# Kernel optimization log

Measured on AMD Instinct MI355X. Metric: run time of the kernel, lower is better.

## Reference

```python
import jax, jax.numpy as jnp
import numpy as np

OUT_C, IN_C, KS, KN = 256, 256, 3, 4
TEMP = 1.0
D1 = OUT_C * KS            # 768
D2 = IN_C * KS             # 768
D2R = D2 // 2 + 1          # 385 (rfft width)


def _freq_indices():
    # mirror torch get_fft2freq(d1, d2, use_rfft=True)
    fh = np.fft.fftfreq(D1)
    fw = np.fft.rfftfreq(D2)
    grid = np.stack(np.meshgrid(fh, fw, indexing='ij'), axis=-1)  # (D1, D2R, 2)
    dist = np.linalg.norm(grid, axis=-1).ravel()
    idx = np.argsort(dist, kind='stable')
    return (idx // D2R).astype(np.int32), (idx % D2R).astype(np.int32)


def setup_inputs() -> dict:
    key = jax.random.key(0)
    k1, k2, k3 = jax.random.split(key, 3)
    b, h, w = 8, 64, 64
    fh, fw = _freq_indices()
    num_freq = fh.shape[0]  # 295680 = D1 * D2R (param_reduction == 1.0)
    return {
        'x': jax.random.normal(k1, (b, IN_C, h, w), dtype=jnp.float32),
        'dft_weight': jax.random.normal(k2, (KN, num_freq, 2), dtype=jnp.float32) * 1e-6,
        'k_att': jax.random.normal(k3, (b, KN, 1, 1), dtype=jnp.float32),
        'freq_h': jnp.asarray(fh),
        'freq_w': jnp.asarray(fw),
    }


def reference(x, dft_weight, k_att, freq_h, freq_w):
    b, c, h, w = x.shape
    # kernel attention: sigmoid(att / temp) * 2 / kernel_num
    att = jax.nn.sigmoid(k_att / TEMP) * (2.0 / KN)          # (b, KN, 1, 1)
    # weighted sum of per-kernel frequency weights -> (b, F, 2)
    wsum = jnp.einsum('knf,bk->bnf', dft_weight, att.reshape(b, KN))
    wc = jax.lax.complex(wsum[..., 0], wsum[..., 1])          # (b, F) complex
    # scatter into dense rfft2 map (indices are a permutation: no duplicates)
    dft_map = jnp.zeros((b, D1, D2R), dtype=jnp.complex64)
    dft_map = dft_map.at[:, freq_h, freq_w].set(wc)
    # inverse rFFT2 -> spatial weights (b, D1, D2)
    sw = jnp.fft.irfft2(dft_map, s=(D1, D2))
    # (b, out, ks, in, ks) -> (b, out, in, ks, ks) -> grouped-conv kernel
    wk = sw.reshape(b, OUT_C, KS, IN_C, KS).transpose(0, 1, 3, 2, 4)
    wk = wk.reshape(b * OUT_C, IN_C, KS, KS)
    # batch of per-sample convs == one grouped conv with groups=b
    xg = x.reshape(1, b * c, h, w)
    out = jax.lax.conv_general_dilated(
        xg, wk, window_strides=(1, 1), padding=[(1, 1), (1, 1)],
        dimension_numbers=('NCHW', 'OIHW', 'NCHW'), feature_group_count=b)
    return out.reshape(b, OUT_C, out.shape[2], out.shape[3])
```

## Files before the change

kernel.cpp:

```cpp
#include <hip/hip_runtime.h>
#include <math.h>

#define D1 768
#define D2R 385
#define NF 295680
#define KNUM 4
#define NB 8
#define NC 256
#define TWOPI_768 0.008181230868723419f

#define ATW_U32 1572864u
#define YA_U32 2752512u
#define T_U32 3981312u
#define SPECB_K_U32 344064u
#define WBF_BYTE 9437184u

typedef __attribute__((ext_vector_type(8))) short short8;
typedef __attribute__((ext_vector_type(16))) float f32x16;
union U4S8 { unsigned int u[4]; uint4 u4; short8 s8; };

static __device__ __forceinline__ unsigned int f2bf(float f) {
  unsigned int u = __float_as_uint(f);
  return (u + 0x7fffu + ((u >> 16) & 1u)) >> 16;
}

__global__ __launch_bounds__(256) void prep_kernel(
    const float* __restrict__ dw, const int* __restrict__ fh,
    const int* __restrict__ fw, unsigned int* __restrict__ ws) {
  long i = (long)blockIdx.x * 256 + threadIdx.x;
  if (i < 1182720) {
    int k = (int)(i / NF);
    int r = (int)(i - (long)k * NF);
    const float2 v = ((const float2*)dw)[i];
    int h = fh[r], c = fw[r];
    ws[(size_t)k * SPECB_K_U32 + (size_t)c * 768 + h] =
        f2bf(v.x) | (f2bf(v.y) << 16);
    return;
  }
  long j = i - 1182720;
  if (j < 1179648) {
    int ri = (int)(j / 589824);
    int rem = (int)(j - (long)ri * 589824);
    int m = rem / 768, h = rem - (rem / 768) * 768;
    int idx = (h * m) % 768;
    float s, c;
    sincosf((float)idx * TWOPI_768, &s, &c);
    unsigned lo, hi;
    if (ri == 0) { lo = f2bf(c); hi = f2bf(-s); }
    else         { lo = f2bf(s); hi = f2bf(c); }
    ws[ATW_U32 + j] = lo | (hi << 16);
  } else if (j < 1486848) {
    long p = j - 1179648;
    int n = (int)(p / 400), cc = (int)(p - (p / 400) * 400);
    unsigned v = 0;
    if (cc <= 384) {
      float wgt = (cc == 0 || cc == 384) ? 1.6954210069444445e-6f
                                         : 3.390842013888889e-6f;
      int idx = (cc * n) % 768;
      float s, c;
      sincosf((float)idx * TWOPI_768, &s, &c);
      v = f2bf(wgt * c) | (f2bf(-wgt * s) << 16);
    }
    ws[T_U32 + (size_t)n * 400 + cc] = v;
  } else if (j < 1680384) {
    long p = j - 1486848;
    int k = (int)(p / 48384);
    long r = p - (long)k * 48384;
    int row = 385 + (int)(r / 768);
    int col = (int)(r - (r / 768) * 768);
    ws[(size_t)k * SPECB_K_U32 + (size_t)row * 768 + col] = 0u;
  } else if (j < 1726464) {
    long p = j - 1680384;
    int k = (int)(p / 11520);
    long r = p - (long)k * 11520;
    int m = (int)(r / 15), jj = (int)(r - (r / 15) * 15);
    ws[YA_U32 + (size_t)k * 307200 + (size_t)m * 400 + 385 + jj] = 0u;
  }
}

__global__ __launch_bounds__(256) void fftA_kernel(
    const unsigned short* __restrict__ Atw,
    const unsigned short* __restrict__ specB,
    unsigned short* __restrict__ Ya) {
  __shared__ __align__(16) unsigned short Al[2][64 * 40], Bl[2][64 * 40];
  int t = threadIdx.x;
  int mt = blockIdx.x, nt = blockIdx.y, z = blockIdx.z;
  int ri = z & 1, k = z >> 1;
  const unsigned short* Ag =
      Atw + (size_t)ri * 1179648 + (size_t)(mt * 64) * 1536;
  const unsigned short* Bg =
      specB + (size_t)k * 688128 + (size_t)(nt * 64) * 1536;
  int rowS = t >> 2, q = t & 3;
  int lane = t & 63, w = t >> 6;
  int moff = (w & 1) * 32, noff = (w >> 1) * 32;
  int lm = lane & 31, half = lane >> 5;
  int wr = rowS * 40 + q * 8;
  int ao = (moff + lm) * 40 + half * 8;
  int bo = (noff + lm) * 40 + half * 8;

  f32x16 acc;
#pragma unroll
  for (int r = 0; r < 16; ++r) acc[r] = 0.f;

  uint4 av = *(const uint4*)(Ag + (size_t)rowS * 1536 + q * 8);
  uint4 bv = *(const uint4*)(Bg + (size_t)rowS * 1536 + q * 8);
  *(uint4*)&Al[0][wr] = av;
  *(uint4*)&Bl[0][wr] = bv;
  __syncthreads();

  for (int kb = 0; kb < 48; ++kb) {
    bool more = (kb < 47);
    if (more) {
      av = *(const uint4*)(Ag + (size_t)rowS * 1536 + (kb + 1) * 32 + q * 8);
      bv = *(const uint4*)(Bg + (size_t)rowS * 1536 + (kb + 1) * 32 + q * 8);
    }
    const unsigned short* Ab = Al[kb & 1];
    const unsigned short* Bb = Bl[kb & 1];
#pragma unroll
    for (int kk2 = 0; kk2 < 2; ++kk2) {
      short8 a8 = *(const short8*)&Ab[ao + kk2 * 16];
      short8 b8 = *(const short8*)&Bb[bo + kk2 * 16];
      acc = __builtin_amdgcn_mfma_f32_32x32x16_bf16(a8, b8, acc, 0, 0, 0);
    }
    if (more) {
      *(uint4*)&Al[(kb + 1) & 1][wr] = av;
      *(uint4*)&Bl[(kb + 1) & 1][wr] = bv;
    }
    __syncthreads();
  }

  int c = nt * 64 + noff + lm;
  if (c < D2R) {
    unsigned short* Yk = Ya + (size_t)k * 614400;
    int mb = mt * 64 + moff + 4 * half;
#pragma unroll
    for (int reg = 0; reg < 16; ++reg) {
      int m = mb + (reg & 3) + 8 * (reg >> 2);
      Yk[(size_t)m * 800 + 2 * c + ri] = (unsigned short)f2bf(acc[reg]);
    }
  }
}

__global__ __launch_bounds__(256) void fftB_kernel(
    const unsigned short* __restrict__ Ya, const unsigned short* __restrict__ T,
    float* __restrict__ SW) {
  __shared__ __align__(16) unsigned short Al[2][64 * 40], Bl[2][64 * 40];
  int t = threadIdx.x;
  int mt = blockIdx.x, nt = blockIdx.y, k = blockIdx.z;
  const unsigned short* Ag = Ya + (size_t)k * 614400 + (size_t)(mt * 64) * 800;
  const unsigned short* Bg = T + (size_t)(nt * 64) * 800;
  int rowS = t >> 2, q = t & 3;
  int lane = t & 63, w = t >> 6;
  int moff = (w & 1) * 32, noff = (w >> 1) * 32;
  int lm = lane & 31, half = lane >> 5;
  int wr = rowS * 40 + q * 8;
  int ao = (moff + lm) * 40 + half * 8;
  int bo = (noff + lm) * 40 + half * 8;

  f32x16 acc;
#pragma unroll
  for (int r = 0; r < 16; ++r) acc[r] = 0.f;

  uint4 av = *(const uint4*)(Ag + (size_t)rowS * 800 + q * 8);
  uint4 bv = *(const uint4*)(Bg + (size_t)rowS * 800 + q * 8);
  *(uint4*)&Al[0][wr] = av;
  *(uint4*)&Bl[0][wr] = bv;
  __syncthreads();

  for (int kb = 0; kb < 25; ++kb) {
    bool more = (kb < 24);
    if (more) {
      av = *(const uint4*)(Ag + (size_t)rowS * 800 + (kb + 1) * 32 + q * 8);
      bv = *(const uint4*)(Bg + (size_t)rowS * 800 + (kb + 1) * 32 + q * 8);
    }
    const unsigned short* Ab = Al[kb & 1];
    const unsigned short* Bb = Bl[kb & 1];
#pragma unroll
    for (int kk2 = 0; kk2 < 2; ++kk2) {
      short8 a8 = *(const short8*)&Ab[ao + kk2 * 16];
      short8 b8 = *(const short8*)&Bb[bo + kk2 * 16];
      acc = __builtin_amdgcn_mfma_f32_32x32x16_bf16(a8, b8, acc, 0, 0, 0);
    }
    if (more) {
      *(uint4*)&Al[(kb + 1) & 1][wr] = av;
      *(uint4*)&Bl[(kb + 1) & 1][wr] = bv;
    }
    __syncthreads();
  }

  float* SWk = SW + (size_t)k * 589824;
  int n = nt * 64 + noff + lm;
  int mb = mt * 64 + moff + 4 * half;
#pragma unroll
  for (int reg = 0; reg < 16; ++reg) {
    int m = mb + (reg & 3) + 8 * (reg >> 2);
    SWk[(size_t)m * 768 + n] = acc[reg];
  }
}

__global__ __launch_bounds__(256) void wprep_kernel(
    const float* __restrict__ ka, const float* __restrict__ SW,
    unsigned short* __restrict__ wBF) {
  int task = blockIdx.x * 256 + threadIdx.x;
  int oc = task & 255;
  int rest = task >> 8;
  int icb = rest & 15;
  int s = rest >> 4;
  int dy = s / 3, dx = s - dy * 3;

  float att[8][4];
#pragma unroll
  for (int b = 0; b < 8; ++b)
#pragma unroll
    for (int k = 0; k < 4; ++k)
      att[b][k] = 0.5f / (1.f + expf(-ka[b * 4 + k]));

  const float* r0 = SW + ((size_t)(oc * 3 + dy)) * D1 + icb * 48 + dx;
  const float* r1 = r0 + 589824;
  const float* r2 = r1 + 589824;
  const float* r3 = r2 + 589824;
  float v0[16], v1[16], v2[16], v3[16];
#pragma unroll
  for (int i = 0; i < 16; ++i) {
    v0[i] = r0[i * 3]; v1[i] = r1[i * 3];
    v2[i] = r2[i * 3]; v3[i] = r3[i * 3];
  }
#pragma unroll
  for (int b = 0; b < 8; ++b) {
    unsigned short ov[16];
#pragma unroll
    for (int i = 0; i < 16; ++i) {
      float v = att[b][0] * v0[i] + att[b][1] * v1[i] + att[b][2] * v2[i] +
                att[b][3] * v3[i];
      ov[i] = (unsigned short)f2bf(v);
    }
    uint4* dst =
        (uint4*)(wBF + ((((size_t)(b * 16 + icb) * 9 + s) * 256 + oc) * 16));
    dst[0] = *(uint4*)&ov[0];
    dst[1] = *(uint4*)&ov[8];
  }
}

__global__ __launch_bounds__(256, 2) void conv_mfma_kernel(
    const float* __restrict__ x, const unsigned short* __restrict__ wBF,
    float* __restrict__ out) {
  __shared__ __align__(16) unsigned char ldsX[2][4 * 66 * 48];
  int t = threadIdx.x;
  int pxt = blockIdx.x, oct = blockIdx.y, b = blockIdx.z;
  int py0 = pxt * 2, oc0 = oct * 128;
  int lane = t & 63, w = t >> 6;
  int ocq = w >> 1, pxq = w & 1;
  int n = lane & 31, half = lane >> 5;

  if (t < 192) {
    int buf = t / 96, r2 = t - buf * 96;
    int site = r2 / 12, word = r2 - site * 12;
    int r = site >> 1, c = (site & 1) ? 65 : 0;
    *(unsigned int*)(&ldsX[buf][(r * 66 + c) * 48 + word * 4]) = 0u;
  }

  f32x16 acc[2][2];
#pragma unroll
  for (int i = 0; i < 2; ++i)
#pragma unroll
    for (int j = 0; j < 2; ++j)
#pragma unroll
      for (int r = 0; r < 16; ++r) acc[i][j][r] = 0.f;

  int s_cq = t >> 5, s_r = (t >> 3) & 3, s_icp = t & 7;
  int iy = py0 - 1 + s_r;
  bool valid = (iy >= 0 && iy < 64);
  const float* xpb =
      x + (((size_t)b * NC) * 64 + (valid ? iy : 0)) * 64 + s_cq * 8;
  int xwoff = (s_r * 66 + 1 + s_cq * 8) * 48 + s_icp * 4;

  const uint4* wg4 = (const uint4*)wBF;
  size_t abase =
      (size_t)b * 144 * 512 + (size_t)(oc0 + ocq * 64 + n) * 2 + half;
  U4S8 pf[3][2];
#pragma unroll
  for (int i = 0; i < 3; ++i) {
    pf[i][0].u4 = wg4[abase + (size_t)i * 512];
    pf[i][1].u4 = wg4[abase + (size_t)i * 512 + 64];
  }

  {
    float4 qa0 = make_float4(0.f, 0.f, 0.f, 0.f), qa1 = qa0, qb0 = qa0,
           qb1 = qa0;
    if (valid) {
      const float* p0 = xpb + (size_t)(s_icp * 2) * 4096;
      qa0 = *(const float4*)p0;
      qa1 = *(const float4*)(p0 + 4);
      qb0 = *(const float4*)(p0 + 4096);
      qb1 = *(const float4*)(p0 + 4100);
    }
    float av[8] = {qa0.x, qa0.y, qa0.z, qa0.w, qa1.x, qa1.y, qa1.z, qa1.w};
    float bv[8] = {qb0.x, qb0.y, qb0.z, qb0.w, qb1.x, qb1.y, qb1.z, qb1.w};
    unsigned char* xw = &ldsX[0][0] + xwoff;
#pragma unroll
    for (int j = 0; j < 8; ++j)
      *(unsigned int*)(xw + j * 48) = f2bf(av[j]) | (f2bf(bv[j]) << 16);
  }
  __syncthreads();

  for (int icb = 0; icb < 16; ++icb) {
    float4 qa0 = make_float4(0.f, 0.f, 0.f, 0.f), qa1 = qa0, qb0 = qa0,
           qb1 = qa0;
    if (icb < 15 && valid) {
      const float* p0 = xpb + ((size_t)(icb + 1) * 16 + s_icp * 2) * 4096;
      qa0 = *(const float4*)p0;
      qa1 = *(const float4*)(p0 + 4);
      qb0 = *(const float4*)(p0 + 4096);
      qb1 = *(const float4*)(p0 + 4100);
    }
    const unsigned char* bufR = &ldsX[icb & 1][0];
#pragma unroll
    for (int s = 0; s < 9; ++s) {
      int step = icb * 9 + s;
      int slot = s % 3;
      int dy = s / 3, dx = s - dy * 3;
      const unsigned char* bb =
          bufR + ((pxq + dy) * 66 + n + dx) * 48 + half * 16;
      short8 B0 = *(const short8*)bb;
      short8 B1 = *(const short8*)(bb + 32 * 48);
      acc[0][0] = __builtin_amdgcn_mfma_f32_32x32x16_bf16(pf[slot][0].s8, B0,
                                                          acc[0][0], 0, 0, 0);
      acc[0][1] = __builtin_amdgcn_mfma_f32_32x32x16_bf16(pf[slot][0].s8, B1,
                                                          acc[0][1], 0, 0, 0);
      acc[1][0] = __builtin_amdgcn_mfma_f32_32x32x16_bf16(pf[slot][1].s8, B0,
                                                          acc[1][0], 0, 0, 0);
      acc[1][1] = __builtin_amdgcn_mfma_f32_32x32x16_bf16(pf[slot][1].s8, B1,
                                                          acc[1][1], 0, 0, 0);
      if (step + 3 < 144) {
        pf[slot][0].u4 = wg4[abase + (size_t)(step + 3) * 512];
        pf[slot][1].u4 = wg4[abase + (size_t)(step + 3) * 512 + 64];
      }
    }
    if (icb < 15) {
      float av[8] = {qa0.x, qa0.y, qa0.z, qa0.w, qa1.x, qa1.y, qa1.z, qa1.w};
      float bv[8] = {qb0.x, qb0.y, qb0.z, qb0.w, qb1.x, qb1.y, qb1.z, qb1.w};
      unsigned char* xw = &ldsX[(icb + 1) & 1][0] + xwoff;
#pragma unroll
      for (int j = 0; j < 8; ++j)
        *(unsigned int*)(xw + j * 48) = f2bf(av[j]) | (f2bf(bv[j]) << 16);
    }
    __syncthreads();
  }

  int py = py0 + pxq;
#pragma unroll
  for (int osub = 0; osub < 2; ++osub)
#pragma unroll
    for (int psub = 0; psub < 2; ++psub) {
      int OC = oc0 + ocq * 64 + osub * 32 + 4 * half;
      int pxc = psub * 32 + n;
      float* op = out + (((size_t)(b * NC + OC)) * 64 + py) * 64 + pxc;
#pragma unroll
      for (int reg = 0; reg < 16; ++reg) {
        int ocm = (reg & 3) + 8 * (reg >> 2);
        op[(size_t)ocm * 4096] = acc[osub][psub][reg];
      }
    }
}

extern "C" void kernel_launch(void* const* d_in, const int* in_sizes, int n_in,
                              void* d_out, int out_size, void* d_ws,
                              size_t ws_size, hipStream_t stream) {
  const float* x = (const float*)d_in[0];
  const float* dw = (const float*)d_in[1];
  const float* ka = (const float*)d_in[2];
  const int* fh = (const int*)d_in[3];
  const int* fw = (const int*)d_in[4];
  float* out = (float*)d_out;
  unsigned int* ws = (unsigned int*)d_ws;
  const unsigned short* specB = (const unsigned short*)d_ws;
  const unsigned short* Atw = (const unsigned short*)((char*)d_ws + 6291456);
  unsigned short* Ya = (unsigned short*)((char*)d_ws + 11010048);
  const unsigned short* T = (const unsigned short*)((char*)d_ws + 15925248);
  float* SW = (float*)d_ws;
  unsigned short* wBF = (unsigned short*)((char*)d_ws + WBF_BYTE);

  hipLaunchKernelGGL(prep_kernel, dim3(11364), dim3(256), 0, stream, dw, fh,
                     fw, ws);
  hipLaunchKernelGGL(fftA_kernel, dim3(12, 7, 8), dim3(256), 0, stream, Atw,
                     specB, Ya);
  hipLaunchKernelGGL(fftB_kernel, dim3(12, 12, KNUM), dim3(256), 0, stream, Ya,
                     T, SW);
  hipLaunchKernelGGL(wprep_kernel, dim3(144), dim3(256), 0, stream, ka, SW,
                     wBF);
  hipLaunchKernelGGL(conv_mfma_kernel, dim3(32, 2, NB), dim3(256), 0, stream,
                     x, wBF, out);
}
```

Before: 200.8 us.

## Shrink conv output tile per wave and restructure wprep via LDS rows

The conv kernel now gives each block 64 output channels instead of 128, so each wave holds 2 MFMA accumulators instead of 4. The grid doubles to 32x4x8 and the launch bound rises to 4 blocks per SM, aiming for more occupancy and latency hiding, at the cost of reloading the input tile from LDS/global twice as often. Separately, wprep_kernel now runs one block per SW row. It stages the four kernel rows in LDS with float4 loads instead of strided per-thread global loads, but writes bf16 outputs as individual 2-byte stores.

```diff
diff --git a/kernel.cpp b/kernel.cpp
--- a/kernel.cpp
+++ b/kernel.cpp
@@ -201,55 +201,49 @@
 __global__ __launch_bounds__(256) void wprep_kernel(
     const float* __restrict__ ka, const float* __restrict__ SW,
     unsigned short* __restrict__ wBF) {
-  int task = blockIdx.x * 256 + threadIdx.x;
-  int oc = task & 255;
-  int rest = task >> 8;
-  int icb = rest & 15;
-  int s = rest >> 4;
-  int dy = s / 3, dx = s - dy * 3;
-
+  __shared__ float rowL[4][768];
+  int t = threadIdx.x;
+  int row = blockIdx.x;
+  int oc = row / 3, dy = row - oc * 3;
+  if (t < 192) {
+#pragma unroll
+    for (int k = 0; k < 4; ++k)
+      *(float4*)&rowL[k][t * 4] =
+          *(const float4*)(SW + (size_t)k * 589824 + (size_t)row * 768 + t * 4);
+  }
   float att[8][4];
 #pragma unroll
   for (int b = 0; b < 8; ++b)
 #pragma unroll
     for (int k = 0; k < 4; ++k)
       att[b][k] = 0.5f / (1.f + expf(-ka[b * 4 + k]));
-
-  const float* r0 = SW + ((size_t)(oc * 3 + dy)) * D1 + icb * 48 + dx;
-  const float* r1 = r0 + 589824;
-  const float* r2 = r1 + 589824;
-  const float* r3 = r2 + 589824;
-  float v0[16], v1[16], v2[16], v3[16];
-#pragma unroll
-  for (int i = 0; i < 16; ++i) {
-    v0[i] = r0[i * 3]; v1[i] = r1[i * 3];
-    v2[i] = r2[i * 3]; v3[i] = r3[i * 3];
-  }
-#pragma unroll
-  for (int b = 0; b < 8; ++b) {
-    unsigned short ov[16];
-#pragma unroll
-    for (int i = 0; i < 16; ++i) {
-      float v = att[b][0] * v0[i] + att[b][1] * v1[i] + att[b][2] * v2[i] +
-                att[b][3] * v3[i];
-      ov[i] = (unsigned short)f2bf(v);
-    }
-    uint4* dst =
-        (uint4*)(wBF + ((((size_t)(b * 16 + icb) * 9 + s) * 256 + oc) * 16));
-    dst[0] = *(uint4*)&ov[0];
-    dst[1] = *(uint4*)&ov[8];
-  }
-}
-
-__global__ __launch_bounds__(256, 2) void conv_mfma_kernel(
+  __syncthreads();
+  int icb = t >> 4, i = t & 15;
+#pragma unroll
+  for (int dx = 0; dx < 3; ++dx) {
+    int col = icb * 48 + dx + 3 * i;
+    float v0 = rowL[0][col], v1 = rowL[1][col], v2 = rowL[2][col],
+          v3 = rowL[3][col];
+    int s = dy * 3 + dx;
+#pragma unroll
+    for (int b = 0; b < 8; ++b) {
+      float v = att[b][0] * v0 + att[b][1] * v1 + att[b][2] * v2 +
+                att[b][3] * v3;
+      wBF[(((size_t)(b * 16 + icb) * 9 + s) * 256 + oc) * 16 + i] =
+          (unsigned short)f2bf(v);
+    }
+  }
+}
+
+__global__ __launch_bounds__(256, 4) void conv_mfma_kernel(
     const float* __restrict__ x, const unsigned short* __restrict__ wBF,
     float* __restrict__ out) {
   __shared__ __align__(16) unsigned char ldsX[2][4 * 66 * 48];
   int t = threadIdx.x;
   int pxt = blockIdx.x, oct = blockIdx.y, b = blockIdx.z;
-  int py0 = pxt * 2, oc0 = oct * 128;
+  int py0 = pxt * 2, oc0 = oct * 64;
   int lane = t & 63, w = t >> 6;
-  int ocq = w >> 1, pxq = w & 1;
+  int pxq = w & 1, pxw = w >> 1;
   int n = lane & 31, half = lane >> 5;
 
   if (t < 192) {
@@ -259,13 +253,11 @@
     *(unsigned int*)(&ldsX[buf][(r * 66 + c) * 48 + word * 4]) = 0u;
   }
 
-  f32x16 acc[2][2];
+  f32x16 acc[2];
 #pragma unroll
   for (int i = 0; i < 2; ++i)
 #pragma unroll
-    for (int j = 0; j < 2; ++j)
-#pragma unroll
-      for (int r = 0; r < 16; ++r) acc[i][j][r] = 0.f;
+    for (int r = 0; r < 16; ++r) acc[i][r] = 0.f;
 
   int s_cq = t >> 5, s_r = (t >> 3) & 3, s_icp = t & 7;
   int iy = py0 - 1 + s_r;
@@ -275,8 +267,7 @@
   int xwoff = (s_r * 66 + 1 + s_cq * 8) * 48 + s_icp * 4;
 
   const uint4* wg4 = (const uint4*)wBF;
-  size_t abase =
-      (size_t)b * 144 * 512 + (size_t)(oc0 + ocq * 64 + n) * 2 + half;
+  size_t abase = (size_t)b * 144 * 512 + (size_t)(oc0 + n) * 2 + half;
   U4S8 pf[3][2];
 #pragma unroll
   for (int i = 0; i < 3; ++i) {
@@ -320,17 +311,12 @@
       int slot = s % 3;
       int dy = s / 3, dx = s - dy * 3;
       const unsigned char* bb =
-          bufR + ((pxq + dy) * 66 + n + dx) * 48 + half * 16;
+          bufR + ((pxq + dy) * 66 + pxw * 32 + n + dx) * 48 + half * 16;
       short8 B0 = *(const short8*)bb;
-      short8 B1 = *(const short8*)(bb + 32 * 48);
-      acc[0][0] = __builtin_amdgcn_mfma_f32_32x32x16_bf16(pf[slot][0].s8, B0,
-                                                          acc[0][0], 0, 0, 0);
-      acc[0][1] = __builtin_amdgcn_mfma_f32_32x32x16_bf16(pf[slot][0].s8, B1,
-                                                          acc[0][1], 0, 0, 0);
-      acc[1][0] = __builtin_amdgcn_mfma_f32_32x32x16_bf16(pf[slot][1].s8, B0,
-                                                          acc[1][0], 0, 0, 0);
-      acc[1][1] = __builtin_amdgcn_mfma_f32_32x32x16_bf16(pf[slot][1].s8, B1,
-                                                          acc[1][1], 0, 0, 0);
+      acc[0] = __builtin_amdgcn_mfma_f32_32x32x16_bf16(pf[slot][0].s8, B0,
+                                                       acc[0], 0, 0, 0);
+      acc[1] = __builtin_amdgcn_mfma_f32_32x32x16_bf16(pf[slot][1].s8, B0,
+                                                       acc[1], 0, 0, 0);
       if (step + 3 < 144) {
         pf[slot][0].u4 = wg4[abase + (size_t)(step + 3) * 512];
         pf[slot][1].u4 = wg4[abase + (size_t)(step + 3) * 512 + 64];
@@ -348,19 +334,17 @@
   }
 
   int py = py0 + pxq;
-#pragma unroll
-  for (int osub = 0; osub < 2; ++osub)
-#pragma unroll
-    for (int psub = 0; psub < 2; ++psub) {
-      int OC = oc0 + ocq * 64 + osub * 32 + 4 * half;
-      int pxc = psub * 32 + n;
-      float* op = out + (((size_t)(b * NC + OC)) * 64 + py) * 64 + pxc;
-#pragma unroll
-      for (int reg = 0; reg < 16; ++reg) {
-        int ocm = (reg & 3) + 8 * (reg >> 2);
-        op[(size_t)ocm * 4096] = acc[osub][psub][reg];
-      }
-    }
+  int pxc = pxw * 32 + n;
+#pragma unroll
+  for (int osub = 0; osub < 2; ++osub) {
+    int OC = oc0 + osub * 32 + 4 * half;
+    float* op = out + (((size_t)(b * NC + OC)) * 64 + py) * 64 + pxc;
+#pragma unroll
+    for (int reg = 0; reg < 16; ++reg) {
+      int ocm = (reg & 3) + 8 * (reg >> 2);
+      op[(size_t)ocm * 4096] = acc[osub][reg];
+    }
+  }
 }
 
 extern "C" void kernel_launch(void* const* d_in, const int* in_sizes, int n_in,
@@ -386,8 +370,8 @@
                      specB, Ya);
   hipLaunchKernelGGL(fftB_kernel, dim3(12, 12, KNUM), dim3(256), 0, stream, Ya,
                      T, SW);
-  hipLaunchKernelGGL(wprep_kernel, dim3(144), dim3(256), 0, stream, ka, SW,
+  hipLaunchKernelGGL(wprep_kernel, dim3(768), dim3(256), 0, stream, ka, SW,
                      wBF);
-  hipLaunchKernelGGL(conv_mfma_kernel, dim3(32, 2, NB), dim3(256), 0, stream,
+  hipLaunchKernelGGL(conv_mfma_kernel, dim3(32, 4, NB), dim3(256), 0, stream,
                      x, wBF, out);
 }
```

Result: slower. 217.0 us (+8.0%).
